# Optimization experiments

Measured on AMD Instinct MI355X. Metric: run time of the kernel, lower is better.

The kernel has to match this reference:

```python
import jax, jax.numpy as jnp
import numpy as np

LN_EPS = 1e-5
C_HID = 16  # c: outer-product channel dim
C_Z = 128


def setup_inputs() -> dict:
    key = jax.random.key(0)
    ks = jax.random.split(key, 4)
    B, N, L, c_m = 1, 128, 512, 256
    c, c_z = C_HID, C_Z
    s_in = 1.0 / np.sqrt(c_m)
    s_out = 1.0 / np.sqrt(c * c)
    return {
        "m": jax.random.normal(ks[0], (B, N, L, c_m), jnp.float32),
        "gamma": jnp.ones((c_m,), jnp.float32),
        "beta": jnp.zeros((c_m,), jnp.float32),
        "Wi": jax.random.normal(ks[1], (c_m, c), jnp.float32) * s_in,
        "bi": jnp.zeros((c,), jnp.float32),
        "Wj": jax.random.normal(ks[2], (c_m, c), jnp.float32) * s_in,
        "bj": jnp.zeros((c,), jnp.float32),
        "Wo": jax.random.normal(ks[3], (c * c, c_z), jnp.float32) * s_out,
        "bo": jnp.zeros((c_z,), jnp.float32),
    }


def reference(m, gamma, beta, Wi, bi, Wj, bj, Wo, bo):
    # LayerNorm over c_m
    mu = jnp.mean(m, axis=-1, keepdims=True)
    var = jnp.mean(jnp.square(m - mu), axis=-1, keepdims=True)
    mn = (m - mu) * jax.lax.rsqrt(var + LN_EPS) * gamma + beta
    # dual projections: (B, N, L, c)
    a = mn @ Wi + bi
    b = mn @ Wj + bj
    # mean over MSA sequences N -> (B, L, c)
    a2 = jnp.mean(a, axis=1)
    b2 = jnp.mean(b, axis=1)
    # outer product + output linear fused:
    # einsum('bic,bjd->bijcd') -> reshape (B,L,L,c*c) -> Linear(c*c -> c_z)
    c = a2.shape[-1]
    Wo3 = Wo.reshape(c, c, -1)  # (c, c, c_z)
    out = jnp.einsum('bic,bjd,cdz->bijz', a2, b2, Wo3) + bo
    return out  # (B, L, L, c_z)
```

## Files before the change

### kernel.cpp

```cpp
#include <hip/hip_runtime.h>


#define LN_EPS 1e-5f

constexpr int N_SEQ = 128;
constexpr int L_DIM = 512;
constexpr int CM    = 256;
constexpr int CH    = 16;
constexpr int CZ    = 128;
constexpr int NPART = 4;

typedef float floatx4 __attribute__((ext_vector_type(4)));

__global__ __launch_bounds__(256) void k1_ln_rowsum(
    const float* __restrict__ m, float* __restrict__ partial)
{
  const int l    = blockIdx.x;
  const int p    = blockIdx.y;
  const int t    = threadIdx.x;
  const int wave = t >> 6;
  const int lane = t & 63;

  float4 v[8];
#pragma unroll
  for (int r = 0; r < 8; ++r) {
    const int n = p * 32 + wave * 8 + r;
    v[r] = *((const float4*)(m + ((size_t)n * L_DIM + l) * CM) + lane);
  }

  float s0 = 0.f, s1 = 0.f, s2 = 0.f, s3 = 0.f;
#pragma unroll
  for (int r = 0; r < 8; ++r) {
    float sum = v[r].x + v[r].y + v[r].z + v[r].w;
    float sq  = v[r].x * v[r].x + v[r].y * v[r].y + v[r].z * v[r].z + v[r].w * v[r].w;
#pragma unroll
    for (int off = 1; off < 64; off <<= 1) {
      sum += __shfl_xor(sum, off, 64);
      sq  += __shfl_xor(sq,  off, 64);
    }
    const float mu   = sum * (1.0f / CM);
    const float var  = sq * (1.0f / CM) - mu * mu;
    const float rstd = rsqrtf(var + LN_EPS);
    s0 += (v[r].x - mu) * rstd;
    s1 += (v[r].y - mu) * rstd;
    s2 += (v[r].z - mu) * rstd;
    s3 += (v[r].w - mu) * rstd;
  }

  __shared__ float sacc[4][CM];
  *((float4*)&sacc[wave][4 * lane]) = make_float4(s0, s1, s2, s3);
  __syncthreads();
  const float s = sacc[0][t] + sacc[1][t] + sacc[2][t] + sacc[3][t];
  partial[((size_t)p * L_DIM + l) * CM + t] = s;
}

__global__ __launch_bounds__(256) void k2_proj(
    const float* __restrict__ partial,
    const float* __restrict__ gamma, const float* __restrict__ beta,
    const float* __restrict__ Wi, const float* __restrict__ bi,
    const float* __restrict__ Wj, const float* __restrict__ bj,
    const float* __restrict__ Wo,
    float* __restrict__ a2, float* __restrict__ T)
{
  const int l = blockIdx.x;
  const int t = threadIdx.x;

  __shared__ float s_lds[CM];
  __shared__ float pacc[32][9];
  __shared__ float ab[32];

  float s = 0.f;
  for (int p = 0; p < NPART; ++p)
    s += partial[((size_t)p * L_DIM + l) * CM + t];
  s = gamma[t] * s + (float)N_SEQ * beta[t];
  s_lds[t] = s;
  __syncthreads();

  const int ch  = t >> 3;
  const int sub = t & 7;
  const int c   = ch & 15;
  const float* __restrict__ W = (ch < CH) ? Wi : Wj;
  float acc = 0.f;
  for (int k = 0; k < 32; ++k) {
    const int e = sub * 32 + k;
    acc += s_lds[e] * W[e * CH + c];
  }
  pacc[ch][sub] = acc;
  __syncthreads();

  if (t < 32) {
    float a = 0.f;
    for (int q = 0; q < 8; ++q) a += pacc[t][q];
    a = a * (1.0f / N_SEQ) + ((t < CH) ? bi[t] : bj[t - CH]);
    ab[t] = a;
    if (t < CH) a2[l * CH + t] = a;
  }
  __syncthreads();

  const int z   = t & (CZ - 1);
  const int chi = t >> 7;
  for (int q = 0; q < 8; ++q) {
    const int cc = chi * 8 + q;
    float accT = 0.f;
#pragma unroll
    for (int d = 0; d < CH; ++d)
      accT += ab[CH + d] * Wo[(cc * CH + d) * CZ + z];
    T[((size_t)l * CH + cc) * CZ + z] = accT;
  }
}

__global__ __launch_bounds__(256) void k3_out(
    const float* __restrict__ a2, const float* __restrict__ T,
    const float* __restrict__ bo, float* __restrict__ out)
{
  const int t  = threadIdx.x;
  const int z4 = t & 31;
  const int j  = blockIdx.x * 8 + (t >> 5);
  const int i0 = blockIdx.y * 32;

  float4 Treg[CH];
  {
    const float4* Tg = (const float4*)T + (size_t)j * (CH * 32) + z4;
#pragma unroll
    for (int c = 0; c < CH; ++c)
      Treg[c] = Tg[c * 32];
  }
  const float4 bov = ((const float4*)bo)[z4];

#define FMA4(av, tv) { acc.x += (av)*(tv).x; acc.y += (av)*(tv).y; \
                       acc.z += (av)*(tv).z; acc.w += (av)*(tv).w; }
  for (int ii = 0; ii < 32; ++ii) {
    const int i = i0 + ii;
    const float4* ar4 = (const float4*)(a2 + (size_t)i * CH);
    const float4 a0 = ar4[0], a1 = ar4[1], a2v = ar4[2], a3 = ar4[3];
    float4 acc = bov;
    FMA4(a0.x, Treg[0]);  FMA4(a0.y, Treg[1]);  FMA4(a0.z, Treg[2]);  FMA4(a0.w, Treg[3]);
    FMA4(a1.x, Treg[4]);  FMA4(a1.y, Treg[5]);  FMA4(a1.z, Treg[6]);  FMA4(a1.w, Treg[7]);
    FMA4(a2v.x, Treg[8]); FMA4(a2v.y, Treg[9]); FMA4(a2v.z, Treg[10]); FMA4(a2v.w, Treg[11]);
    FMA4(a3.x, Treg[12]); FMA4(a3.y, Treg[13]); FMA4(a3.z, Treg[14]); FMA4(a3.w, Treg[15]);
    floatx4* dst = (floatx4*)(out + ((size_t)i * L_DIM + j) * CZ) + z4;
    floatx4 accv = { acc.x, acc.y, acc.z, acc.w };
    __builtin_nontemporal_store(accv, dst);
  }
#undef FMA4
}

extern "C" void kernel_launch(void* const* d_in, const int* in_sizes, int n_in,
                              void* d_out, int out_size, void* d_ws, size_t ws_size,
                              hipStream_t stream) {
  const float* m     = (const float*)d_in[0];
  const float* gamma = (const float*)d_in[1];
  const float* beta  = (const float*)d_in[2];
  const float* Wi    = (const float*)d_in[3];
  const float* bi    = (const float*)d_in[4];
  const float* Wj    = (const float*)d_in[5];
  const float* bj    = (const float*)d_in[6];
  const float* Wo    = (const float*)d_in[7];
  const float* bo    = (const float*)d_in[8];
  float* out = (float*)d_out;

  char* ws = (char*)d_ws;
  float* partial = (float*)ws;
  float* a2      = (float*)(ws + (size_t)NPART * L_DIM * CM * 4);
  float* T       = (float*)(ws + (size_t)NPART * L_DIM * CM * 4
                               + (size_t)L_DIM * CH * 4);

  k1_ln_rowsum<<<dim3(L_DIM, NPART), 256, 0, stream>>>(m, partial);
  k2_proj<<<dim3(L_DIM), 256, 0, stream>>>(partial, gamma, beta,
                                           Wi, bi, Wj, bj, Wo, a2, T);
  k3_out<<<dim3(64, 16), 256, 0, stream>>>(a2, T, bo, out);
}
```

Measured before the change: 214.4 us.

## Fuse LayerNorm row-sum into projection kernel and enlarge output tile per block

Merges the LayerNorm/row-sum kernel into the projection kernel. Each of 512 blocks now processes all 128 sequences for one column l, so the partial-sum workspace round trip and one launch go away. The output kernel's blocks now each cover 64 rows of i instead of 32, halving the grid and reusing the register-held T tile longer. The cost is fewer blocks in the memory-heavy first stage (512 instead of 2048), which may lower occupancy and latency hiding while streaming the 64MB input.

```diff
diff --git a/kernel.cpp b/kernel.cpp
--- a/kernel.cpp
+++ b/kernel.cpp
@@ -8,72 +8,58 @@
 constexpr int CM    = 256;
 constexpr int CH    = 16;
 constexpr int CZ    = 128;
-constexpr int NPART = 4;
 
 typedef float floatx4 __attribute__((ext_vector_type(4)));
 
-__global__ __launch_bounds__(256) void k1_ln_rowsum(
-    const float* __restrict__ m, float* __restrict__ partial)
-{
-  const int l    = blockIdx.x;
-  const int p    = blockIdx.y;
-  const int t    = threadIdx.x;
-  const int wave = t >> 6;
-  const int lane = t & 63;
-
-  float4 v[8];
-#pragma unroll
-  for (int r = 0; r < 8; ++r) {
-    const int n = p * 32 + wave * 8 + r;
-    v[r] = *((const float4*)(m + ((size_t)n * L_DIM + l) * CM) + lane);
-  }
-
-  float s0 = 0.f, s1 = 0.f, s2 = 0.f, s3 = 0.f;
-#pragma unroll
-  for (int r = 0; r < 8; ++r) {
-    float sum = v[r].x + v[r].y + v[r].z + v[r].w;
-    float sq  = v[r].x * v[r].x + v[r].y * v[r].y + v[r].z * v[r].z + v[r].w * v[r].w;
-#pragma unroll
-    for (int off = 1; off < 64; off <<= 1) {
-      sum += __shfl_xor(sum, off, 64);
-      sq  += __shfl_xor(sq,  off, 64);
-    }
-    const float mu   = sum * (1.0f / CM);
-    const float var  = sq * (1.0f / CM) - mu * mu;
-    const float rstd = rsqrtf(var + LN_EPS);
-    s0 += (v[r].x - mu) * rstd;
-    s1 += (v[r].y - mu) * rstd;
-    s2 += (v[r].z - mu) * rstd;
-    s3 += (v[r].w - mu) * rstd;
-  }
-
-  __shared__ float sacc[4][CM];
-  *((float4*)&sacc[wave][4 * lane]) = make_float4(s0, s1, s2, s3);
-  __syncthreads();
-  const float s = sacc[0][t] + sacc[1][t] + sacc[2][t] + sacc[3][t];
-  partial[((size_t)p * L_DIM + l) * CM + t] = s;
-}
-
-__global__ __launch_bounds__(256) void k2_proj(
-    const float* __restrict__ partial,
+__global__ __launch_bounds__(256) void kA_ln_proj(
+    const float* __restrict__ m,
     const float* __restrict__ gamma, const float* __restrict__ beta,
     const float* __restrict__ Wi, const float* __restrict__ bi,
     const float* __restrict__ Wj, const float* __restrict__ bj,
     const float* __restrict__ Wo,
     float* __restrict__ a2, float* __restrict__ T)
 {
-  const int l = blockIdx.x;
-  const int t = threadIdx.x;
+  const int l    = blockIdx.x;
+  const int t    = threadIdx.x;
+  const int wave = t >> 6;
+  const int lane = t & 63;
 
+  float s0 = 0.f, s1 = 0.f, s2 = 0.f, s3 = 0.f;
+  for (int rb = 0; rb < 4; ++rb) {
+    float4 v[8];
+#pragma unroll
+    for (int r = 0; r < 8; ++r) {
+      const int n = wave * 32 + rb * 8 + r;
+      v[r] = *((const float4*)(m + ((size_t)n * L_DIM + l) * CM) + lane);
+    }
+#pragma unroll
+    for (int r = 0; r < 8; ++r) {
+      float sum = v[r].x + v[r].y + v[r].z + v[r].w;
+      float sq  = v[r].x * v[r].x + v[r].y * v[r].y + v[r].z * v[r].z + v[r].w * v[r].w;
+#pragma unroll
+      for (int off = 1; off < 64; off <<= 1) {
+        sum += __shfl_xor(sum, off, 64);
+        sq  += __shfl_xor(sq,  off, 64);
+      }
+      const float mu   = sum * (1.0f / CM);
+      const float var  = sq * (1.0f / CM) - mu * mu;
+      const float rstd = rsqrtf(var + LN_EPS);
+      s0 += (v[r].x - mu) * rstd;
+      s1 += (v[r].y - mu) * rstd;
+      s2 += (v[r].z - mu) * rstd;
+      s3 += (v[r].w - mu) * rstd;
+    }
+  }
+
+  __shared__ float sacc[4][CM];
   __shared__ float s_lds[CM];
   __shared__ float pacc[32][9];
   __shared__ float ab[32];
 
-  float s = 0.f;
-  for (int p = 0; p < NPART; ++p)
-    s += partial[((size_t)p * L_DIM + l) * CM + t];
-  s = gamma[t] * s + (float)N_SEQ * beta[t];
-  s_lds[t] = s;
+  *((float4*)&sacc[wave][4 * lane]) = make_float4(s0, s1, s2, s3);
+  __syncthreads();
+  s_lds[t] = gamma[t] * (sacc[0][t] + sacc[1][t] + sacc[2][t] + sacc[3][t])
+           + (float)N_SEQ * beta[t];
   __syncthreads();
 
   const int ch  = t >> 3;
@@ -109,14 +95,14 @@
   }
 }
 
-__global__ __launch_bounds__(256) void k3_out(
+__global__ __launch_bounds__(256) void kB_out(
     const float* __restrict__ a2, const float* __restrict__ T,
     const float* __restrict__ bo, float* __restrict__ out)
 {
   const int t  = threadIdx.x;
   const int z4 = t & 31;
   const int j  = blockIdx.x * 8 + (t >> 5);
-  const int i0 = blockIdx.y * 32;
+  const int i0 = blockIdx.y * 64;
 
   float4 Treg[CH];
   {
@@ -129,7 +115,8 @@
 
 #define FMA4(av, tv) { acc.x += (av)*(tv).x; acc.y += (av)*(tv).y; \
                        acc.z += (av)*(tv).z; acc.w += (av)*(tv).w; }
-  for (int ii = 0; ii < 32; ++ii) {
+#pragma unroll 2
+  for (int ii = 0; ii < 64; ++ii) {
     const int i = i0 + ii;
     const float4* ar4 = (const float4*)(a2 + (size_t)i * CH);
     const float4 a0 = ar4[0], a1 = ar4[1], a2v = ar4[2], a3 = ar4[3];
@@ -160,13 +147,10 @@
   float* out = (float*)d_out;
 
   char* ws = (char*)d_ws;
-  float* partial = (float*)ws;
-  float* a2      = (float*)(ws + (size_t)NPART * L_DIM * CM * 4);
-  float* T       = (float*)(ws + (size_t)NPART * L_DIM * CM * 4
-                               + (size_t)L_DIM * CH * 4);
+  float* a2 = (float*)ws;
+  float* T  = (float*)(ws + (size_t)L_DIM * CH * 4);
 
-  k1_ln_rowsum<<<dim3(L_DIM, NPART), 256, 0, stream>>>(m, partial);
-  k2_proj<<<dim3(L_DIM), 256, 0, stream>>>(partial, gamma, beta,
-                                           Wi, bi, Wj, bj, Wo, a2, T);
-  k3_out<<<dim3(64, 16), 256, 0, stream>>>(a2, T, bo, out);
+  kA_ln_proj<<<dim3(L_DIM), 256, 0, stream>>>(m, gamma, beta,
+                                              Wi, bi, Wj, bj, Wo, a2, T);
+  kB_out<<<dim3(64, 8), 256, 0, stream>>>(a2, T, bo, out);
 }
```

Measured after the change: 210.5 us. About the same (-1.9%).
